# Optimization experiments

Measured on AMD Instinct MI355X. Metric: run time of the kernel, lower is better.

The kernel has to match this reference:

```python
import jax, jax.numpy as jnp
import numpy as np

VOCAB, EMB, HID, LAYERS = 32000, 512, 512, 2
B, S = 16, 256


def setup_inputs() -> dict:
    key = jax.random.key(0)
    ks = jax.random.split(key, 8)
    x = jax.random.randint(ks[0], (B, S), 0, VOCAB)
    emb = jax.random.normal(ks[1], (VOCAB, EMB), dtype=jnp.float32) * 0.02
    # input_dim == hidden_dim == 512, so per-layer weights can be stacked
    Wih = jax.random.normal(ks[2], (LAYERS, 4 * HID, EMB), dtype=jnp.float32) * 0.05
    Whh = jax.random.normal(ks[3], (LAYERS, 4 * HID, HID), dtype=jnp.float32) * 0.05
    b = jax.random.normal(ks[4], (LAYERS, 4 * HID), dtype=jnp.float32) * 0.05
    fc_w = jax.random.normal(ks[5], (VOCAB, HID), dtype=jnp.float32) * 0.02
    fc_b = jnp.zeros((VOCAB,), dtype=jnp.float32)
    return {"x": x, "emb": emb, "Wih": Wih, "Whh": Whh, "b": b, "fc_w": fc_w, "fc_b": fc_b}


def reference(x, emb, Wih, Whh, b, fc_w, fc_b):
    L = Wih.shape[0]
    Bsz = x.shape[0]
    H = Whh.shape[-1]
    xe = emb[x]  # (B, S, E)
    h0 = jnp.zeros((L, Bsz, H), dtype=emb.dtype)
    c0 = jnp.zeros((L, Bsz, H), dtype=emb.dtype)

    def step(carry, xt):  # xt: (B, E)
        h, c = carry
        inp = xt
        hs, cs = [], []
        for l in range(L):  # small fixed layer loop
            gates = inp @ Wih[l].T + h[l] @ Whh[l].T + b[l]  # (B, 4H)
            i, f, g, o = jnp.split(gates, 4, axis=1)
            cn = jax.nn.sigmoid(f) * c[l] + jax.nn.sigmoid(i) * jnp.tanh(g)
            hn = jax.nn.sigmoid(o) * jnp.tanh(cn)
            hs.append(hn)
            cs.append(cn)
            inp = hn
        return (jnp.stack(hs), jnp.stack(cs)), inp

    _, outs = jax.lax.scan(step, (h0, c0), jnp.swapaxes(xe, 0, 1))  # outs: (S, B, H)
    outs = jnp.swapaxes(outs, 0, 1)  # (B, S, H); dropout is identity (eval)
    logits = outs @ fc_w.T + fc_b  # (B, S, V)
    return logits
```

## Files before the change

### kernel.cpp

```cpp
#include <hip/hip_runtime.h>
#include <hip/hip_bf16.h>

#define SEQ 256
#define NB 16
#define HID 512
#define VOC 32000

typedef short bf16x8 __attribute__((ext_vector_type(8)));
typedef float f32x4 __attribute__((ext_vector_type(4)));
typedef unsigned long long u64;

__device__ __forceinline__ void ld_lds16(const void* g, void* l) {
  __builtin_amdgcn_global_load_lds((const __attribute__((address_space(1))) void*)g,
                                   (__attribute__((address_space(3))) void*)l, 16, 0, 0);
}

__device__ __forceinline__ float sigf(float x) { return 1.0f / (1.0f + expf(-x)); }

__device__ __forceinline__ unsigned pk2(float a, float b) {
  __hip_bfloat16 ha = __float2bfloat16(a), hb = __float2bfloat16(b);
  unsigned short ua = *(unsigned short*)&ha, ub = *(unsigned short*)&hb;
  return (unsigned)ua | ((unsigned)ub << 16);
}

__device__ __forceinline__ u64 agload(const u64* p) {
  return __hip_atomic_load(p, __ATOMIC_RELAXED, __HIP_MEMORY_SCOPE_AGENT);
}
__device__ __forceinline__ void agstore(u64* p, u64 v) {
  __hip_atomic_store(p, v, __ATOMIC_RELAXED, __HIP_MEMORY_SCOPE_AGENT);
}

template <int N>
__device__ __forceinline__ void issueN(u64* q, const u64* base) {
#pragma unroll
  for (int i = 0; i < N; ++i) q[i] = agload(base + (i >> 2) * 256 + (i & 3) * 16);
}
template <int N>
__device__ __forceinline__ void revalN(u64* q, const u64* base, unsigned tg) {
  for (;;) {
    int bad = 0;
#pragma unroll
    for (int i = 0; i < N; ++i) bad |= ((unsigned)(q[i] >> 32) != tg);
    if (!__any(bad)) break;
    __builtin_amdgcn_s_sleep(1);
#pragma unroll
    for (int i = 0; i < N; ++i)
      if ((unsigned)(q[i] >> 32) != tg) q[i] = agload(base + (i >> 2) * 256 + (i & 3) * 16);
  }
}

__device__ __forceinline__ void cvt8_hilo(const float* p, bf16x8* h8, bf16x8* l8) {
  union { unsigned short u[8]; bf16x8 v; } uh, ul;
#pragma unroll
  for (int i = 0; i < 8; ++i) {
    float v = p[i];
    __hip_bfloat16 h = __float2bfloat16(v);
    uh.u[i] = *(unsigned short*)&h;
    float rem = v - __bfloat162float(h);
    __hip_bfloat16 l = __float2bfloat16(rem);
    ul.u[i] = *(unsigned short*)&l;
  }
  *h8 = uh.v;
  *l8 = ul.v;
}

__global__ void embed_k(const int* __restrict__ x, const float* __restrict__ emb,
                        unsigned short* __restrict__ xe) {
  int bid = blockIdx.x;
  int t = bid >> 4, b = bid & 15;
  int tok = x[b * SEQ + t];
  const float4* src = (const float4*)(emb + (size_t)tok * HID);
  int e = threadIdx.x;
  float4 a = src[e * 2], c = src[e * 2 + 1];
  uint4 o;
  o.x = pk2(a.x, a.y); o.y = pk2(a.z, a.w);
  o.z = pk2(c.x, c.y); o.w = pk2(c.z, c.w);
  ((uint4*)(xe + (size_t)bid * HID))[e] = o;
}

__global__ void cvt_k(const float* __restrict__ in, uint4* __restrict__ out) {
  size_t i = (size_t)blockIdx.x * blockDim.x + threadIdx.x;
  const float4* in4 = (const float4*)in;
  float4 a = in4[i * 2], b = in4[i * 2 + 1];
  uint4 o;
  o.x = pk2(a.x, a.y); o.y = pk2(a.z, a.w);
  o.z = pk2(b.x, b.y); o.w = pk2(b.z, b.w);
  out[i] = o;
}

__global__ __launch_bounds__(256) void gx_gemm(const __hip_bfloat16* __restrict__ A,
                                               const __hip_bfloat16* __restrict__ Bw,
                                               unsigned short* __restrict__ C) {
  __shared__ __align__(16) unsigned short lds_a[128 * 32];
  __shared__ __align__(16) unsigned short lds_b[128 * 32];
  const int tid = threadIdx.x;
  const int lane = tid & 63, wid = tid >> 6;
  const int m0 = blockIdx.y * 128, n0 = blockIdx.x * 128;
  const char* Ab = (const char*)A;
  const char* Bb = (const char*)Bw;
  const int ra = tid >> 2, cb = (tid & 3) * 16;
  f32x4 acc[4][4] = {};
  const int wm = (wid >> 1) * 64, wn = (wid & 1) * 64;
  const int fr = lane & 15, fk = (lane >> 4) * 8;
  for (int k0 = 0; k0 < HID; k0 += 32) {
    ld_lds16(Ab + (size_t)(m0 + ra) * 1024 + k0 * 2 + cb, (char*)lds_a + wid * 1024);
    ld_lds16(Ab + (size_t)(m0 + 64 + ra) * 1024 + k0 * 2 + cb, (char*)lds_a + 4096 + wid * 1024);
    ld_lds16(Bb + (size_t)(n0 + ra) * 1024 + k0 * 2 + cb, (char*)lds_b + wid * 1024);
    ld_lds16(Bb + (size_t)(n0 + 64 + ra) * 1024 + k0 * 2 + cb, (char*)lds_b + 4096 + wid * 1024);
    __syncthreads();
    bf16x8 af[4], bf[4];
#pragma unroll
    for (int i = 0; i < 4; ++i) af[i] = *(const bf16x8*)&lds_a[(wm + i * 16 + fr) * 32 + fk];
#pragma unroll
    for (int j = 0; j < 4; ++j) bf[j] = *(const bf16x8*)&lds_b[(wn + j * 16 + fr) * 32 + fk];
#pragma unroll
    for (int i = 0; i < 4; ++i)
#pragma unroll
      for (int j = 0; j < 4; ++j)
        acc[i][j] = __builtin_amdgcn_mfma_f32_16x16x32_bf16(af[i], bf[j], acc[i][j], 0, 0, 0);
    __syncthreads();
  }
  const int cr = (lane >> 4) * 4, cc = lane & 15;
#pragma unroll
  for (int i = 0; i < 4; ++i)
#pragma unroll
    for (int jj = 0; jj < 4; ++jj) {
      size_t base = (size_t)(m0 + wm + i * 16 + cr) * 2048 + (n0 + wn + jj * 16 + cc);
#pragma unroll
      for (int r = 0; r < 4; ++r) {
        __hip_bfloat16 h = __float2bfloat16(acc[i][jj][r]);
        C[base + (size_t)r * 2048] = *(unsigned short*)&h;
      }
    }
}

__global__ __launch_bounds__(512, 1) void lstm_k(
    const float* __restrict__ Wih, const float* __restrict__ Whh,
    const float* __restrict__ bias, const unsigned short* __restrict__ gxb,
    u64* __restrict__ h0r, u64* __restrict__ h1r, unsigned short* __restrict__ outs) {
  const int bid = blockIdx.x;
  const int sel = bid & 7;
  if (sel > 1) return;
  const int lay = sel, r = bid >> 3;
  const int hc0 = r * 16;
  const int tid = threadIdx.x;
  const int wv = tid >> 6, lane = tid & 63;
  const int b16 = lane & 15, hi = lane >> 4;
  __shared__ float pbuf[8][64][17];

  bf16x8 W[4][2][4];
  {
    const int q = b16 >> 2, c = b16 & 3;
    if (lay == 0) {
#pragma unroll
      for (int m = 0; m < 4; ++m) {
        const float* row = Whh + (size_t)(q * HID + hc0 + m * 4 + c) * HID;
#pragma unroll
        for (int s = 0; s < 2; ++s)
          cvt8_hilo(row + wv * 64 + s * 32 + hi * 8, &W[m][0][s], &W[m][1][s]);
      }
    } else {
      const float* basep = (wv < 4) ? Wih : Whh;
      const int kb = (wv & 3) * 128;
#pragma unroll
      for (int m = 0; m < 4; ++m) {
        const float* row = basep + (size_t)(2048 + q * HID + hc0 + m * 4 + c) * HID;
#pragma unroll
        for (int s = 0; s < 4; ++s)
          cvt8_hilo(row + kb + s * 32 + hi * 8, &W[m][0][s], &W[m][1][s]);
      }
    }
  }
  const int eb = b16, ehl = hi;
  const bool epi = (wv < 4);
  float bq[4];
  if (epi) {
#pragma unroll
    for (int q = 0; q < 4; ++q) bq[q] = bias[lay * 2048 + q * HID + hc0 + wv * 4 + ehl];
  }
  float c_reg = 0.f;

#pragma unroll 1
  for (int t = 0; t < SEQ; ++t) {
    f32x4 acc[4] = {{0.f, 0.f, 0.f, 0.f}, {0.f, 0.f, 0.f, 0.f},
                    {0.f, 0.f, 0.f, 0.f}, {0.f, 0.f, 0.f, 0.f}};
    float gxr[4] = {0.f, 0.f, 0.f, 0.f};
    if (lay == 0) {
      const u64* src = h0r + (size_t)t * 4096 + (wv * 512 + hi * 64 + b16);
      u64 q8[8];
      issueN<8>(q8, src);
      if (epi) {
        const unsigned short* gp = gxb + ((size_t)(t * 16 + eb)) * 2048 + hc0 + wv * 4 + ehl;
#pragma unroll
        for (int q = 0; q < 4; ++q) {
          union { unsigned u; float f; } cv;
          cv.u = (unsigned)gp[q * HID] << 16;
          gxr[q] = cv.f;
          asm volatile("" : "+v"(gxr[q]));
        }
      }
      revalN<8>(q8, src, (unsigned)t);
#pragma unroll
      for (int s = 0; s < 2; ++s) {
        union { unsigned u[4]; bf16x8 v; } bb;
#pragma unroll
        for (int j = 0; j < 4; ++j) bb.u[j] = (unsigned)q8[s * 4 + j];
#pragma unroll
        for (int m = 0; m < 4; ++m) {
          acc[m] = __builtin_amdgcn_mfma_f32_16x16x32_bf16(W[m][0][s], bb.v, acc[m], 0, 0, 0);
          acc[m] = __builtin_amdgcn_mfma_f32_16x16x32_bf16(W[m][1][s], bb.v, acc[m], 0, 0, 0);
        }
      }
    } else {
      const u64* src = ((wv < 4) ? (h0r + (size_t)(t + 1) * 4096)
                                 : (h1r + (size_t)t * 4096))
                       + ((wv & 3) * 1024 + hi * 64 + b16);
      const unsigned tg = (wv < 4) ? (unsigned)(t + 1) : (unsigned)t;
      u64 q16[16];
      issueN<16>(q16, src);
      revalN<16>(q16, src, tg);
#pragma unroll
      for (int s = 0; s < 4; ++s) {
        union { unsigned u[4]; bf16x8 v; } bb;
#pragma unroll
        for (int j = 0; j < 4; ++j) bb.u[j] = (unsigned)q16[s * 4 + j];
#pragma unroll
        for (int m = 0; m < 4; ++m) {
          acc[m] = __builtin_amdgcn_mfma_f32_16x16x32_bf16(W[m][0][s], bb.v, acc[m], 0, 0, 0);
          acc[m] = __builtin_amdgcn_mfma_f32_16x16x32_bf16(W[m][1][s], bb.v, acc[m], 0, 0, 0);
        }
      }
    }
#pragma unroll
    for (int m = 0; m < 4; ++m)
#pragma unroll
      for (int rr = 0; rr < 4; ++rr) pbuf[wv][m * 16 + hi * 4 + rr][b16] = acc[m][rr];
    __syncthreads();

    if (epi) {
      float pre[4];
#pragma unroll
      for (int q = 0; q < 4; ++q) {
        const int rl = wv * 16 + q * 4 + ehl;
        float s0 = pbuf[0][rl][eb] + pbuf[1][rl][eb] + pbuf[2][rl][eb] + pbuf[3][rl][eb];
        float s1 = pbuf[4][rl][eb] + pbuf[5][rl][eb] + pbuf[6][rl][eb] + pbuf[7][rl][eb];
        pre[q] = bq[q] + gxr[q] + s0 + s1;
      }
      float iv = sigf(pre[0]), fv = sigf(pre[1]);
      float gv = tanhf(pre[2]), ov = sigf(pre[3]);
      c_reg = fv * c_reg + iv * gv;
      float hn = ov * tanhf(c_reg);
      __hip_bfloat16 hh = __float2bfloat16(hn);
      int hb = (int)*(unsigned short*)&hh;
      int pr = __shfl_xor(hb, 16, 64);
      unsigned data32 = (unsigned)(unsigned short)hb | ((unsigned)(unsigned short)pr << 16);
      u64 tagw = (u64)(unsigned)(t + 1) << 32;
      u64* ringo = (lay ? h1r : h0r) + (size_t)(t + 1) * 4096;
      if ((ehl & 1) == 0) {
        const int cp = r * 8 + wv * 2 + (ehl >> 1);
        agstore(ringo + cp * 16 + eb, (u64)data32 | tagw);
      }
      if (lay) {
        unsigned d2 = (unsigned)__shfl((int)data32, eb + 32, 64);
        if (ehl == 0)
          *(u64*)(outs + ((size_t)(t * 16 + eb)) * 512 + hc0 + wv * 4) =
              (u64)data32 | ((u64)d2 << 32);
      }
    }
    __syncthreads();
  }
}

__global__ __launch_bounds__(256) void fc_gemm(const __hip_bfloat16* __restrict__ A,
                                               const __hip_bfloat16* __restrict__ Bw,
                                               const float* __restrict__ bias,
                                               float* __restrict__ C) {
  __shared__ __align__(16) unsigned short lds_a[128 * 32];
  __shared__ __align__(16) unsigned short lds_b[128 * 32];
  const int tid = threadIdx.x;
  const int lane = tid & 63, wid = tid >> 6;
  const int m0 = blockIdx.y * 128, n0 = blockIdx.x * 128;
  const char* Ab = (const char*)A;
  const char* Bb = (const char*)Bw;
  const int ra = tid >> 2, cb = (tid & 3) * 16;
  f32x4 acc[4][4] = {};
  const int wm = (wid >> 1) * 64, wn = (wid & 1) * 64;
  const int fr = lane & 15, fk = (lane >> 4) * 8;
  for (int k0 = 0; k0 < HID; k0 += 32) {
    ld_lds16(Ab + (size_t)(m0 + ra) * 1024 + k0 * 2 + cb, (char*)lds_a + wid * 1024);
    ld_lds16(Ab + (size_t)(m0 + 64 + ra) * 1024 + k0 * 2 + cb, (char*)lds_a + 4096 + wid * 1024);
    ld_lds16(Bb + (size_t)(n0 + ra) * 1024 + k0 * 2 + cb, (char*)lds_b + wid * 1024);
    ld_lds16(Bb + (size_t)(n0 + 64 + ra) * 1024 + k0 * 2 + cb, (char*)lds_b + 4096 + wid * 1024);
    __syncthreads();
    bf16x8 af[4], bf[4];
#pragma unroll
    for (int i = 0; i < 4; ++i) af[i] = *(const bf16x8*)&lds_a[(wm + i * 16 + fr) * 32 + fk];
#pragma unroll
    for (int j = 0; j < 4; ++j) bf[j] = *(const bf16x8*)&lds_b[(wn + j * 16 + fr) * 32 + fk];
#pragma unroll
    for (int i = 0; i < 4; ++i)
#pragma unroll
      for (int j = 0; j < 4; ++j)
        acc[i][j] = __builtin_amdgcn_mfma_f32_16x16x32_bf16(af[i], bf[j], acc[i][j], 0, 0, 0);
    __syncthreads();
  }
  const int cr = (lane >> 4) * 4, cc = lane & 15;
  float bv[4];
#pragma unroll
  for (int jj = 0; jj < 4; ++jj) bv[jj] = bias[n0 + wn + jj * 16 + cc];
#pragma unroll
  for (int i = 0; i < 4; ++i) {
#pragma unroll
    for (int jj = 0; jj < 4; ++jj) {
#pragma unroll
      for (int rr = 0; rr < 4; ++rr) {
        int tok = m0 + wm + i * 16 + cr + rr;
        int orow = (tok & 15) * SEQ + (tok >> 4);
        C[(size_t)orow * VOC + (n0 + wn + jj * 16 + cc)] = acc[i][jj][rr] + bv[jj];
      }
    }
  }
}

extern "C" void kernel_launch(void* const* d_in, const int* in_sizes, int n_in,
                              void* d_out, int out_size, void* d_ws, size_t ws_size,
                              hipStream_t stream) {
  const int* x = (const int*)d_in[0];
  const float* emb = (const float*)d_in[1];
  const float* Wih = (const float*)d_in[2];
  const float* Whh = (const float*)d_in[3];
  const float* bias = (const float*)d_in[4];
  const float* fcw = (const float*)d_in[5];
  const float* fcb = (const float*)d_in[6];
  float* out = (float*)d_out;
  char* ws = (char*)d_ws;

  u64* h0r = (u64*)ws;
  u64* h1r = (u64*)(ws + 8421376);
  uint4* wih0_bf = (uint4*)(ws + 16842752);
  unsigned short* gxb = (unsigned short*)(ws + 18939904);
  unsigned short* xe = (unsigned short*)(ws + 35717120);
  unsigned short* outs = (unsigned short*)(ws + 35717120);
  uint4* fcw_bf = (uint4*)ws;

  hipMemsetAsync(ws, 0, 16842752, stream);
  embed_k<<<SEQ * NB, 64, 0, stream>>>(x, emb, xe);
  cvt_k<<<512, 256, 0, stream>>>(Wih, wih0_bf);
  gx_gemm<<<dim3(16, 32), 256, 0, stream>>>((const __hip_bfloat16*)xe,
                                            (const __hip_bfloat16*)wih0_bf, gxb);
  lstm_k<<<256, 512, 0, stream>>>(Wih, Whh, bias, gxb, h0r, h1r, outs);
  cvt_k<<<8000, 256, 0, stream>>>(fcw, fcw_bf);
  fc_gemm<<<dim3(250, 32), 256, 0, stream>>>((const __hip_bfloat16*)outs,
                                             (const __hip_bfloat16*)fcw_bf, fcb, out);
}
```

Before: 1.282 ms.

## Restructure LSTM recurrence with per-wave full-K MFMA and local-ring sc0 polling

Each LSTM wave now covers the full K=512 reduction for four hidden columns, which removes the cross-wave LDS reduction and the barrier in layer 0 and halves the waves in use there. Hidden-state exchange is written both to a small local ring, polled with sc0 loads, and to a fabric-scope ring used as the fallback, which aims to shorten inter-block handoff latency. Layer 1 splits the Wih and Whh work across wave pairs and combines them through a small LDS buffer. The workspace layout is reorganised around the new rings. Relying on sc0 loads for coherence across CUs is risky, and it depends on the fallback path to make progress.

```diff
diff --git a/kernel.cpp b/kernel.cpp
--- a/kernel.cpp
+++ b/kernel.cpp
@@ -5,6 +5,7 @@
 #define NB 16
 #define HID 512
 #define VOC 32000
+#define RSL 16
 
 typedef short bf16x8 __attribute__((ext_vector_type(8)));
 typedef float f32x4 __attribute__((ext_vector_type(4)));
@@ -30,22 +31,45 @@
   __hip_atomic_store(p, v, __ATOMIC_RELAXED, __HIP_MEMORY_SCOPE_AGENT);
 }
 
-template <int N>
-__device__ __forceinline__ void issueN(u64* q, const u64* base) {
-#pragma unroll
-  for (int i = 0; i < N; ++i) q[i] = agload(base + (i >> 2) * 256 + (i & 3) * 16);
-}
-template <int N>
-__device__ __forceinline__ void revalN(u64* q, const u64* base, unsigned tg) {
-  for (;;) {
-    int bad = 0;
-#pragma unroll
-    for (int i = 0; i < N; ++i) bad |= ((unsigned)(q[i] >> 32) != tg);
-    if (!__any(bad)) break;
+__device__ __forceinline__ u64 ld_sc0(const u64* p) {
+  u64 v;
+  asm volatile("global_load_dwordx2 %0, %1, off sc0" : "=v"(v) : "v"(p));
+  return v;
+}
+__device__ __forceinline__ void waitv0() {
+  asm volatile("s_waitcnt vmcnt(0)" ::: "memory");
+  __builtin_amdgcn_sched_barrier(0);
+}
+
+__device__ __forceinline__ void load32_sc0(u64* q, const u64* base) {
+#pragma unroll
+  for (int i = 0; i < 32; ++i) q[i] = ld_sc0(base + (i >> 2) * 256 + (i & 3) * 16);
+  waitv0();
+}
+__device__ __forceinline__ void load32_ag(u64* q, const u64* base) {
+#pragma unroll
+  for (int i = 0; i < 32; ++i) q[i] = agload(base + (i >> 2) * 256 + (i & 3) * 16);
+}
+__device__ __forceinline__ bool ok32(const u64* q, unsigned tg) {
+  int bad = 0;
+#pragma unroll
+  for (int i = 0; i < 32; ++i) bad |= ((unsigned)(q[i] >> 32) != tg);
+  return !__any(bad);
+}
+__device__ __forceinline__ void pollLF32(u64* q, const u64* loc, const u64* fab, unsigned tg) {
+  load32_sc0(q, loc);
+  int rnd = 0;
+  while (!ok32(q, tg)) {
     __builtin_amdgcn_s_sleep(1);
-#pragma unroll
-    for (int i = 0; i < N; ++i)
-      if ((unsigned)(q[i] >> 32) != tg) q[i] = agload(base + (i >> 2) * 256 + (i & 3) * 16);
+    if ((++rnd & 7) == 0) load32_ag(q, fab);
+    else load32_sc0(q, loc);
+  }
+}
+__device__ __forceinline__ void pollF32(u64* q, const u64* fab, unsigned tg) {
+  load32_ag(q, fab);
+  while (!ok32(q, tg)) {
+    __builtin_amdgcn_s_sleep(2);
+    load32_ag(q, fab);
   }
 }
 
@@ -120,132 +144,88 @@
         acc[i][j] = __builtin_amdgcn_mfma_f32_16x16x32_bf16(af[i], bf[j], acc[i][j], 0, 0, 0);
     __syncthreads();
   }
-  const int cr = (lane >> 4) * 4, cc = lane & 15;
+  const int cr = (lane >> 4) * 4, cc2 = lane & 15;
 #pragma unroll
   for (int i = 0; i < 4; ++i)
 #pragma unroll
     for (int jj = 0; jj < 4; ++jj) {
-      size_t base = (size_t)(m0 + wm + i * 16 + cr) * 2048 + (n0 + wn + jj * 16 + cc);
-#pragma unroll
-      for (int r = 0; r < 4; ++r) {
-        __hip_bfloat16 h = __float2bfloat16(acc[i][jj][r]);
-        C[base + (size_t)r * 2048] = *(unsigned short*)&h;
-      }
-    }
-}
-
-__global__ __launch_bounds__(512, 1) void lstm_k(
+      size_t base = (size_t)(m0 + wm + i * 16 + cr) * 2048 + (n0 + wn + jj * 16 + cc2);
+#pragma unroll
+      for (int rr = 0; rr < 4; ++rr) {
+        __hip_bfloat16 h = __float2bfloat16(acc[i][jj][rr]);
+        C[base + (size_t)rr * 2048] = *(unsigned short*)&h;
+      }
+    }
+}
+
+__global__ __launch_bounds__(512, 2) void lstm_k(
     const float* __restrict__ Wih, const float* __restrict__ Whh,
     const float* __restrict__ bias, const unsigned short* __restrict__ gxb,
-    u64* __restrict__ h0r, u64* __restrict__ h1r, unsigned short* __restrict__ outs) {
+    u64* __restrict__ h0loc, u64* __restrict__ h1loc,
+    u64* __restrict__ h0fab, u64* __restrict__ h1fab,
+    unsigned short* __restrict__ outs) {
   const int bid = blockIdx.x;
-  const int sel = bid & 7;
-  if (sel > 1) return;
-  const int lay = sel, r = bid >> 3;
-  const int hc0 = r * 16;
+  const int sel = bid & 7, r = bid >> 3;
   const int tid = threadIdx.x;
   const int wv = tid >> 6, lane = tid & 63;
   const int b16 = lane & 15, hi = lane >> 4;
-  __shared__ float pbuf[8][64][17];
-
-  bf16x8 W[4][2][4];
-  {
-    const int q = b16 >> 2, c = b16 & 3;
-    if (lay == 0) {
-#pragma unroll
-      for (int m = 0; m < 4; ++m) {
-        const float* row = Whh + (size_t)(q * HID + hc0 + m * 4 + c) * HID;
-#pragma unroll
-        for (int s = 0; s < 2; ++s)
-          cvt8_hilo(row + wv * 64 + s * 32 + hi * 8, &W[m][0][s], &W[m][1][s]);
-      }
-    } else {
-      const float* basep = (wv < 4) ? Wih : Whh;
-      const int kb = (wv & 3) * 128;
-#pragma unroll
-      for (int m = 0; m < 4; ++m) {
-        const float* row = basep + (size_t)(2048 + q * HID + hc0 + m * 4 + c) * HID;
-#pragma unroll
-        for (int s = 0; s < 4; ++s)
-          cvt8_hilo(row + kb + s * 32 + hi * 8, &W[m][0][s], &W[m][1][s]);
-      }
-    }
-  }
-  const int eb = b16, ehl = hi;
-  const bool epi = (wv < 4);
-  float bq[4];
-  if (epi) {
-#pragma unroll
-    for (int q = 0; q < 4; ++q) bq[q] = bias[lay * 2048 + q * HID + hc0 + wv * 4 + ehl];
-  }
-  float c_reg = 0.f;
-
+  const int qg = b16 & 3, cc = b16 >> 2;
+  __shared__ __align__(16) float pb[4][64][4];
+
+  if (sel == 0 && r < 32) {
+    if (wv >= 4) return;
+    const int hc0w = r * 16 + wv * 4;
+    bf16x8 Wh[2][16];
+    {
+      const float* wrow = Whh + (size_t)(qg * HID + hc0w + cc) * HID;
+#pragma unroll
+      for (int ks = 0; ks < 16; ++ks)
+        cvt8_hilo(wrow + ks * 32 + hi * 8, &Wh[0][ks], &Wh[1][ks]);
+    }
+    float bq[4];
+#pragma unroll
+    for (int qq = 0; qq < 4; ++qq) bq[qq] = bias[qq * HID + hc0w + hi];
+    float c_reg = 0.f;
+    const int lbase = hi * 64 + b16;
+    u64 qa[32];
 #pragma unroll 1
-  for (int t = 0; t < SEQ; ++t) {
-    f32x4 acc[4] = {{0.f, 0.f, 0.f, 0.f}, {0.f, 0.f, 0.f, 0.f},
-                    {0.f, 0.f, 0.f, 0.f}, {0.f, 0.f, 0.f, 0.f}};
-    float gxr[4] = {0.f, 0.f, 0.f, 0.f};
-    if (lay == 0) {
-      const u64* src = h0r + (size_t)t * 4096 + (wv * 512 + hi * 64 + b16);
-      u64 q8[8];
-      issueN<8>(q8, src);
-      if (epi) {
-        const unsigned short* gp = gxb + ((size_t)(t * 16 + eb)) * 2048 + hc0 + wv * 4 + ehl;
-#pragma unroll
-        for (int q = 0; q < 4; ++q) {
+    for (int t = 0; t < SEQ; ++t) {
+      float gxr[4];
+      {
+        const unsigned short* gp = gxb + (size_t)(t * 16 + b16) * 2048 + hc0w + hi;
+#pragma unroll
+        for (int qq = 0; qq < 4; ++qq) {
           union { unsigned u; float f; } cv;
-          cv.u = (unsigned)gp[q * HID] << 16;
-          gxr[q] = cv.f;
-          asm volatile("" : "+v"(gxr[q]));
+          cv.u = (unsigned)gp[qq * HID] << 16;
+          gxr[qq] = cv.f;
+          asm volatile("" : "+v"(gxr[qq]));
         }
       }
-      revalN<8>(q8, src, (unsigned)t);
-#pragma unroll
-      for (int s = 0; s < 2; ++s) {
-        union { unsigned u[4]; bf16x8 v; } bb;
-#pragma unroll
-        for (int j = 0; j < 4; ++j) bb.u[j] = (unsigned)q8[s * 4 + j];
-#pragma unroll
-        for (int m = 0; m < 4; ++m) {
-          acc[m] = __builtin_amdgcn_mfma_f32_16x16x32_bf16(W[m][0][s], bb.v, acc[m], 0, 0, 0);
-          acc[m] = __builtin_amdgcn_mfma_f32_16x16x32_bf16(W[m][1][s], bb.v, acc[m], 0, 0, 0);
+      const u64* loc = h0loc + (size_t)(t & (RSL - 1)) * 4096 + lbase;
+      const u64* fab = h0fab + (size_t)t * 4096 + lbase;
+      f32x4 a0 = {0.f, 0.f, 0.f, 0.f}, a1 = a0, a2 = a0, a3 = a0;
+#pragma unroll 1
+      for (int h = 0; h < 2; ++h) {
+        pollLF32(qa, loc + h * 2048, fab + h * 2048, (unsigned)t);
+#pragma unroll
+        for (int k2 = 0; k2 < 8; ++k2) {
+          union { unsigned u[4]; bf16x8 v; } bb;
+#pragma unroll
+          for (int j = 0; j < 4; ++j) bb.u[j] = (unsigned)qa[k2 * 4 + j];
+          const int ks = h * 8 + k2;
+          if (k2 & 1) {
+            a2 = __builtin_amdgcn_mfma_f32_16x16x32_bf16(Wh[0][ks], bb.v, a2, 0, 0, 0);
+            a3 = __builtin_amdgcn_mfma_f32_16x16x32_bf16(Wh[1][ks], bb.v, a3, 0, 0, 0);
+          } else {
+            a0 = __builtin_amdgcn_mfma_f32_16x16x32_bf16(Wh[0][ks], bb.v, a0, 0, 0, 0);
+            a1 = __builtin_amdgcn_mfma_f32_16x16x32_bf16(Wh[1][ks], bb.v, a1, 0, 0, 0);
+          }
         }
       }
-    } else {
-      const u64* src = ((wv < 4) ? (h0r + (size_t)(t + 1) * 4096)
-                                 : (h1r + (size_t)t * 4096))
-                       + ((wv & 3) * 1024 + hi * 64 + b16);
-      const unsigned tg = (wv < 4) ? (unsigned)(t + 1) : (unsigned)t;
-      u64 q16[16];
-      issueN<16>(q16, src);
-      revalN<16>(q16, src, tg);
-#pragma unroll
-      for (int s = 0; s < 4; ++s) {
-        union { unsigned u[4]; bf16x8 v; } bb;
-#pragma unroll
-        for (int j = 0; j < 4; ++j) bb.u[j] = (unsigned)q16[s * 4 + j];
-#pragma unroll
-        for (int m = 0; m < 4; ++m) {
-          acc[m] = __builtin_amdgcn_mfma_f32_16x16x32_bf16(W[m][0][s], bb.v, acc[m], 0, 0, 0);
-          acc[m] = __builtin_amdgcn_mfma_f32_16x16x32_bf16(W[m][1][s], bb.v, acc[m], 0, 0, 0);
-        }
-      }
-    }
-#pragma unroll
-    for (int m = 0; m < 4; ++m)
-#pragma unroll
-      for (int rr = 0; rr < 4; ++rr) pbuf[wv][m * 16 + hi * 4 + rr][b16] = acc[m][rr];
-    __syncthreads();
-
-    if (epi) {
+      f32x4 acc = (a0 + a2) + (a1 + a3);
       float pre[4];
 #pragma unroll
-      for (int q = 0; q < 4; ++q) {
-        const int rl = wv * 16 + q * 4 + ehl;
-        float s0 = pbuf[0][rl][eb] + pbuf[1][rl][eb] + pbuf[2][rl][eb] + pbuf[3][rl][eb];
-        float s1 = pbuf[4][rl][eb] + pbuf[5][rl][eb] + pbuf[6][rl][eb] + pbuf[7][rl][eb];
-        pre[q] = bq[q] + gxr[q] + s0 + s1;
-      }
+      for (int qq = 0; qq < 4; ++qq) pre[qq] = bq[qq] + gxr[qq] + acc[qq];
       float iv = sigf(pre[0]), fv = sigf(pre[1]);
       float gv = tanhf(pre[2]), ov = sigf(pre[3]);
       c_reg = fv * c_reg + iv * gv;
@@ -253,21 +233,85 @@
       __hip_bfloat16 hh = __float2bfloat16(hn);
       int hb = (int)*(unsigned short*)&hh;
       int pr = __shfl_xor(hb, 16, 64);
-      unsigned data32 = (unsigned)(unsigned short)hb | ((unsigned)(unsigned short)pr << 16);
-      u64 tagw = (u64)(unsigned)(t + 1) << 32;
-      u64* ringo = (lay ? h1r : h0r) + (size_t)(t + 1) * 4096;
-      if ((ehl & 1) == 0) {
-        const int cp = r * 8 + wv * 2 + (ehl >> 1);
-        agstore(ringo + cp * 16 + eb, (u64)data32 | tagw);
-      }
-      if (lay) {
-        unsigned d2 = (unsigned)__shfl((int)data32, eb + 32, 64);
-        if (ehl == 0)
-          *(u64*)(outs + ((size_t)(t * 16 + eb)) * 512 + hc0 + wv * 4) =
-              (u64)data32 | ((u64)d2 << 32);
-      }
-    }
-    __syncthreads();
+      unsigned d32 = (unsigned)(unsigned short)hb | ((unsigned)(unsigned short)pr << 16);
+      u64 val = (u64)d32 | ((u64)(unsigned)(t + 1) << 32);
+      if ((hi & 1) == 0) {
+        const int cp = (hc0w + hi) >> 1;
+        *(volatile u64*)(h0loc + (size_t)((t + 1) & (RSL - 1)) * 4096 + cp * 16 + b16) = val;
+        agstore(h0fab + (size_t)(t + 1) * 4096 + cp * 16 + b16, val);
+      }
+    }
+  } else if (sel == 1 && r < 32) {
+    const int tt = wv >> 1;
+    const bool whh = (wv & 1) != 0;
+    const int hc0t = r * 16 + tt * 4;
+    bf16x8 W[2][16];
+    {
+      const float* wrow = (whh ? Whh : Wih) + (size_t)(2048 + qg * HID + hc0t + cc) * HID;
+#pragma unroll
+      for (int ks = 0; ks < 16; ++ks)
+        cvt8_hilo(wrow + ks * 32 + hi * 8, &W[0][ks], &W[1][ks]);
+    }
+    float bq[4];
+#pragma unroll
+    for (int qq = 0; qq < 4; ++qq) bq[qq] = bias[2048 + qq * HID + hc0t + hi];
+    float c_reg = 0.f;
+    const int lbase = hi * 64 + b16;
+    u64 qa[32];
+#pragma unroll 1
+    for (int t = 0; t < SEQ; ++t) {
+      f32x4 a0 = {0.f, 0.f, 0.f, 0.f}, a1 = a0, a2 = a0, a3 = a0;
+      const unsigned tg = whh ? (unsigned)t : (unsigned)(t + 1);
+      const u64* fab = (whh ? (h1fab + (size_t)t * 4096)
+                            : (h0fab + (size_t)(t + 1) * 4096)) + lbase;
+      const u64* loc = h1loc + (size_t)(t & (RSL - 1)) * 4096 + lbase;
+#pragma unroll 1
+      for (int h = 0; h < 2; ++h) {
+        if (whh) pollLF32(qa, loc + h * 2048, fab + h * 2048, tg);
+        else pollF32(qa, fab + h * 2048, tg);
+#pragma unroll
+        for (int k2 = 0; k2 < 8; ++k2) {
+          union { unsigned u[4]; bf16x8 v; } bb;
+#pragma unroll
+          for (int j = 0; j < 4; ++j) bb.u[j] = (unsigned)qa[k2 * 4 + j];
+          const int ks = h * 8 + k2;
+          if (k2 & 1) {
+            a2 = __builtin_amdgcn_mfma_f32_16x16x32_bf16(W[0][ks], bb.v, a2, 0, 0, 0);
+            a3 = __builtin_amdgcn_mfma_f32_16x16x32_bf16(W[1][ks], bb.v, a3, 0, 0, 0);
+          } else {
+            a0 = __builtin_amdgcn_mfma_f32_16x16x32_bf16(W[0][ks], bb.v, a0, 0, 0, 0);
+            a1 = __builtin_amdgcn_mfma_f32_16x16x32_bf16(W[1][ks], bb.v, a1, 0, 0, 0);
+          }
+        }
+      }
+      f32x4 acc = (a0 + a2) + (a1 + a3);
+      if (whh) *(f32x4*)&pb[tt][lane][0] = acc;
+      __syncthreads();
+      if (!whh) {
+        f32x4 part = *(f32x4*)&pb[tt][lane][0];
+        float pre[4];
+#pragma unroll
+        for (int qq = 0; qq < 4; ++qq) pre[qq] = bq[qq] + acc[qq] + part[qq];
+        float iv = sigf(pre[0]), fv = sigf(pre[1]);
+        float gv = tanhf(pre[2]), ov = sigf(pre[3]);
+        c_reg = fv * c_reg + iv * gv;
+        float hn = ov * tanhf(c_reg);
+        __hip_bfloat16 hh = __float2bfloat16(hn);
+        int hb = (int)*(unsigned short*)&hh;
+        int pr = __shfl_xor(hb, 16, 64);
+        unsigned d32 = (unsigned)(unsigned short)hb | ((unsigned)(unsigned short)pr << 16);
+        u64 val = (u64)d32 | ((u64)(unsigned)(t + 1) << 32);
+        if ((hi & 1) == 0) {
+          const int cp = (hc0t + hi) >> 1;
+          *(volatile u64*)(h1loc + (size_t)((t + 1) & (RSL - 1)) * 4096 + cp * 16 + b16) = val;
+          agstore(h1fab + (size_t)(t + 1) * 4096 + cp * 16 + b16, val);
+        }
+        unsigned d23 = (unsigned)__shfl((int)d32, b16 + 32, 64);
+        if (hi == 0)
+          *(u64*)(outs + (size_t)(t * 16 + b16) * 512 + hc0t) = (u64)d32 | ((u64)d23 << 32);
+      }
+      __syncthreads();
+    }
   }
 }
 
@@ -304,10 +348,10 @@
         acc[i][j] = __builtin_amdgcn_mfma_f32_16x16x32_bf16(af[i], bf[j], acc[i][j], 0, 0, 0);
     __syncthreads();
   }
-  const int cr = (lane >> 4) * 4, cc = lane & 15;
+  const int cr = (lane >> 4) * 4, cc2 = lane & 15;
   float bv[4];
 #pragma unroll
-  for (int jj = 0; jj < 4; ++jj) bv[jj] = bias[n0 + wn + jj * 16 + cc];
+  for (int jj = 0; jj < 4; ++jj) bv[jj] = bias[n0 + wn + jj * 16 + cc2];
 #pragma unroll
   for (int i = 0; i < 4; ++i) {
 #pragma unroll
@@ -316,7 +360,7 @@
       for (int rr = 0; rr < 4; ++rr) {
         int tok = m0 + wm + i * 16 + cr + rr;
         int orow = (tok & 15) * SEQ + (tok >> 4);
-        C[(size_t)orow * VOC + (n0 + wn + jj * 16 + cc)] = acc[i][jj][rr] + bv[jj];
+        C[(size_t)orow * VOC + (n0 + wn + jj * 16 + cc2)] = acc[i][jj][rr] + bv[jj];
       }
     }
   }
@@ -335,20 +379,22 @@
   float* out = (float*)d_out;
   char* ws = (char*)d_ws;
 
-  u64* h0r = (u64*)ws;
-  u64* h1r = (u64*)(ws + 8421376);
-  uint4* wih0_bf = (uint4*)(ws + 16842752);
-  unsigned short* gxb = (unsigned short*)(ws + 18939904);
-  unsigned short* xe = (unsigned short*)(ws + 35717120);
-  unsigned short* outs = (unsigned short*)(ws + 35717120);
-  uint4* fcw_bf = (uint4*)ws;
-
-  hipMemsetAsync(ws, 0, 16842752, stream);
+  unsigned short* xe = (unsigned short*)ws;
+  unsigned short* outs = (unsigned short*)ws;
+  u64* h0loc = (u64*)(ws + 4194304);
+  u64* h1loc = (u64*)(ws + 4718592);
+  u64* h0fab = (u64*)(ws + 5242880);
+  u64* h1fab = (u64*)(ws + 13664256);
+  uint4* wih0_bf = (uint4*)(ws + 22085632);
+  unsigned short* gxb = (unsigned short*)(ws + 24182784);
+  uint4* fcw_bf = (uint4*)(ws + 4194304);
+
+  hipMemsetAsync(ws + 4194304, 0, 17891328, stream);
   embed_k<<<SEQ * NB, 64, 0, stream>>>(x, emb, xe);
   cvt_k<<<512, 256, 0, stream>>>(Wih, wih0_bf);
   gx_gemm<<<dim3(16, 32), 256, 0, stream>>>((const __hip_bfloat16*)xe,
                                             (const __hip_bfloat16*)wih0_bf, gxb);
-  lstm_k<<<256, 512, 0, stream>>>(Wih, Whh, bias, gxb, h0r, h1r, outs);
+  lstm_k<<<256, 512, 0, stream>>>(Wih, Whh, bias, gxb, h0loc, h1loc, h0fab, h1fab, outs);
   cvt_k<<<8000, 256, 0, stream>>>(fcw, fcw_bf);
   fc_gemm<<<dim3(250, 32), 256, 0, stream>>>((const __hip_bfloat16*)outs,
                                              (const __hip_bfloat16*)fcw_bf, fcb, out);
```

Result: slower. 4.833 ms (+276.9%).
